# Kernel tuning notes

Hardware: AMD Instinct MI355X
Metric: run time of the kernel (lower is better)

The kernel has to match this reference:

```python
import jax, jax.numpy as jnp
import numpy as np

B, S = 256, 32          # sequence layout for the final (b, s, 1) reshape
BATCH = B * S           # 8192 flattened rows processed per call
IN, U, OUT = 32, 128, 1 # sensory inputs, interneurons, motor outputs
UNFOLDS = 6             # semi-implicit ODE solver unfolds


def _syn_sigmoid(v, mu, sigma):
    # v: [B, P]; mu, sigma: [P, Q] -> [B, P, Q] per-synapse gate
    return jax.nn.sigmoid(sigma * (v[:, :, None] - mu))


def setup_inputs() -> dict:
    key = jax.random.key(0)
    ks = jax.random.split(key, 12)
    inputs = jax.random.normal(ks[0], (BATCH, IN), dtype=jnp.float32)
    state = jax.random.normal(ks[1], (BATCH, U), dtype=jnp.float32)
    # adjacency in {-1, 0, 1} (wiring polarity), baked into W / erev as in _get_variables
    sens_adj = jax.random.randint(ks[2], (IN, U), -1, 2).astype(jnp.float32)
    adj = jax.random.randint(ks[3], (U, U), -1, 2).astype(jnp.float32)
    sensory_mu = jax.random.uniform(ks[4], (IN, U)) * 0.5 + 0.3
    sensory_sigma = jax.random.uniform(ks[5], (IN, U)) * 5.0 + 3.0
    # NOTE: original applies +w_init_min OUTSIDE the |adj| mask; reproduced faithfully
    sensory_W = jnp.abs(sens_adj) * jax.random.uniform(ks[6], (IN, U)) * 0.9 + 0.1
    sensory_erev = sens_adj  # erev_init_factor = 1
    mu = jax.random.uniform(ks[7], (U, U)) * 0.5 + 0.3
    sigma = jax.random.uniform(ks[8], (U, U)) * 5.0 + 3.0
    W = jnp.abs(adj) * jax.random.uniform(ks[9], (U, U)) * 0.9 + 0.1
    erev = adj
    vleak = jax.random.uniform(ks[10], (U,)) * 0.4 - 0.2
    gleak = jnp.ones((U,), jnp.float32)        # gleak_init_min == gleak_init_max == 1
    cm_t = jnp.ones((U,), jnp.float32) * 0.5    # cm_init_min == cm_init_max == 0.5
    in_w = jnp.ones((IN,), jnp.float32)         # affine input mapping (init ones/zeros)
    in_b = jnp.zeros((IN,), jnp.float32)
    out_w = jnp.ones((OUT,), jnp.float32)       # affine output mapping
    out_b = jnp.zeros((OUT,), jnp.float32)
    return dict(inputs=inputs, state=state, sensory_mu=sensory_mu,
                sensory_sigma=sensory_sigma, sensory_W=sensory_W,
                sensory_erev=sensory_erev, mu=mu, sigma=sigma, W=W, erev=erev,
                vleak=vleak, gleak=gleak, cm_t=cm_t, in_w=in_w, in_b=in_b,
                out_w=out_w, out_b=out_b, b=B, s=S)


def reference(inputs, state, sensory_mu, sensory_sigma, sensory_W, sensory_erev,
              mu, sigma, W, erev, vleak, gleak, cm_t, in_w, in_b, out_w, out_b,
              b, s):
    x = inputs * in_w + in_b                                   # _map_inputs (Affine)
    # sensory synapse activations, computed once: [BATCH, IN, U]
    sa = sensory_W * _syn_sigmoid(x, sensory_mu, sensory_sigma)
    w_num_s = jnp.sum(sa * sensory_erev, axis=1)               # [BATCH, U]
    w_den_s = jnp.sum(sa, axis=1)                              # [BATCH, U]

    def step(v, _):
        wa = W * _syn_sigmoid(v, mu, sigma)                    # [BATCH, U, U]
        w_num = jnp.sum(wa * erev, axis=1) + w_num_s
        w_den = jnp.sum(wa, axis=1) + w_den_s
        v_new = (cm_t * v + gleak * vleak + w_num) / (cm_t + gleak + w_den)
        return v_new, None

    v, _ = jax.lax.scan(step, state, None, length=UNFOLDS)
    outputs = (v[:, :OUT] * out_w + out_b).reshape(b, s, 1)    # _map_outputs
    return outputs, v
```

## Files before the change

kernel.cpp:

```cpp
#include <hip/hip_runtime.h>

#define NIN 32
#define NU  128
#define RPB 8
#define NQ  4
#define UNFOLDS 6
#define LOG2E 1.44269504088896340736f

typedef float float4v __attribute__((ext_vector_type(4)));

#define SPN (NIN * NU)
#define RPN (NU * NU)

__global__ void pack_params(const float* __restrict__ mu,
                            const float* __restrict__ sig,
                            const float* __restrict__ W,
                            const float* __restrict__ erev,
                            float4v* __restrict__ out, int n) {
    int idx = blockIdx.x * blockDim.x + threadIdx.x;
    if (idx < n) {
        float sg = sig[idx];
        float s2 = -LOG2E * sg;
        float sm2 = -s2 * mu[idx];
        float Wv = W[idx];
        float We = Wv * erev[idx];
        out[idx] = (float4v){s2, sm2, We, Wv};
    }
}

__global__ __launch_bounds__(512, 8)
void wormnet_main(const float* __restrict__ inputs,
                  const float* __restrict__ state,
                  const float4v* __restrict__ sp,
                  const float4v* __restrict__ rp,
                  const float* __restrict__ vleak,
                  const float* __restrict__ gleak,
                  const float* __restrict__ cm_t,
                  const float* __restrict__ in_w, const float* __restrict__ in_b,
                  const float* __restrict__ out_w, const float* __restrict__ out_b,
                  float* __restrict__ out_y,
                  float* __restrict__ out_v)
{
    __shared__ __align__(16) float xs[NIN * RPB];
    __shared__ __align__(16) float vs[NU * RPB];
    __shared__ float rn[RPB][NQ][NU];
    __shared__ float rd[RPB][NQ][NU];

    const int tid  = threadIdx.x;
    const int j    = tid & (NU - 1);
    const int q    = tid >> 7;
    const int base = blockIdx.x * RPB;
    const int u0   = q * 2;

    if (tid < NIN * RPB) {
        int i = tid & (NIN - 1);
        int r = tid >> 5;
        xs[i * RPB + r] = inputs[(base + r) * NIN + i] * in_w[i] + in_b[i];
    }
    float vold[2];
    #pragma unroll
    for (int k = 0; k < 2; ++k) {
        float v = state[(base + u0 + k) * NU + j];
        vold[k] = v;
        vs[j * RPB + u0 + k] = v;
    }
    __syncthreads();

    float numS[RPB], denS[RPB];
    #pragma unroll
    for (int r = 0; r < RPB; ++r) { numS[r] = 0.0f; denS[r] = 0.0f; }
    {
        const float4v* pp = sp + q * (NIN / NQ) * NU + j;
        #pragma unroll 2
        for (int ii = 0; ii < NIN / NQ; ++ii) {
            const int i = q * (NIN / NQ) + ii;
            float4v p = pp[0]; pp += NU;
            float4v xa = *(const float4v*)&xs[i * RPB];
            float4v xb = *(const float4v*)&xs[i * RPB + 4];
            float a[RPB];
            #pragma unroll
            for (int r = 0; r < 4; ++r) {
                a[r]     = 1.0f + __builtin_amdgcn_exp2f(__builtin_fmaf(p.x, xa[r], p.y));
                a[r + 4] = 1.0f + __builtin_amdgcn_exp2f(__builtin_fmaf(p.x, xb[r], p.y));
            }
            #pragma unroll
            for (int w = 0; w < RPB / 2; ++w) {
                float rq = __builtin_amdgcn_rcpf(a[2*w] * a[2*w+1]);
                float s0 = rq * a[2*w+1];
                float s1 = rq * a[2*w];
                numS[2*w]   = __builtin_fmaf(p.z, s0, numS[2*w]);
                denS[2*w]   = __builtin_fmaf(p.w, s0, denS[2*w]);
                numS[2*w+1] = __builtin_fmaf(p.z, s1, numS[2*w+1]);
                denS[2*w+1] = __builtin_fmaf(p.w, s1, denS[2*w+1]);
            }
        }
    }

    const float cm = cm_t[j];
    const float gl = gleak[j];
    const float glvl = gl * vleak[j];
    const float cg = cm + gl;

    for (int u = 0; u < UNFOLDS; ++u) {
        float num[RPB], den[RPB];
        #pragma unroll
        for (int r = 0; r < RPB; ++r) { num[r] = numS[r]; den[r] = denS[r]; }

        const float4v* pp = rp + q * (NU / NQ) * NU + j;
        #pragma unroll 2
        for (int ii = 0; ii < NU / NQ; ++ii) {
            const int i = q * (NU / NQ) + ii;
            float4v p = pp[0]; pp += NU;
            float4v va = *(const float4v*)&vs[i * RPB];
            float4v vb = *(const float4v*)&vs[i * RPB + 4];
            float a[RPB];
            #pragma unroll
            for (int r = 0; r < 4; ++r) {
                a[r]     = 1.0f + __builtin_amdgcn_exp2f(__builtin_fmaf(p.x, va[r], p.y));
                a[r + 4] = 1.0f + __builtin_amdgcn_exp2f(__builtin_fmaf(p.x, vb[r], p.y));
            }
            #pragma unroll
            for (int w = 0; w < RPB / 2; ++w) {
                float rq = __builtin_amdgcn_rcpf(a[2*w] * a[2*w+1]);
                float s0 = rq * a[2*w+1];
                float s1 = rq * a[2*w];
                num[2*w]   = __builtin_fmaf(p.z, s0, num[2*w]);
                den[2*w]   = __builtin_fmaf(p.w, s0, den[2*w]);
                num[2*w+1] = __builtin_fmaf(p.z, s1, num[2*w+1]);
                den[2*w+1] = __builtin_fmaf(p.w, s1, den[2*w+1]);
            }
        }

        #pragma unroll
        for (int r = 0; r < RPB; ++r) {
            rn[r][q][j] = num[r];
            rd[r][q][j] = den[r];
        }
        __syncthreads();

        #pragma unroll
        for (int k = 0; k < 2; ++k) {
            const int r = u0 + k;
            float tn = rn[r][0][j] + rn[r][1][j] + rn[r][2][j] + rn[r][3][j];
            float td = rd[r][0][j] + rd[r][1][j] + rd[r][2][j] + rd[r][3][j];
            float vn = (__builtin_fmaf(cm, vold[k], glvl) + tn)
                       * __builtin_amdgcn_rcpf(cg + td);
            vold[k] = vn;
            vs[j * RPB + r] = vn;
        }
        __syncthreads();
    }

    #pragma unroll
    for (int k = 0; k < 2; ++k) {
        out_v[(base + u0 + k) * NU + j] = vold[k];
    }
    if (j == 0) {
        const float ow = out_w[0], ob = out_b[0];
        #pragma unroll
        for (int k = 0; k < 2; ++k) {
            out_y[base + u0 + k] = __builtin_fmaf(vold[k], ow, ob);
        }
    }
}

extern "C" void kernel_launch(void* const* d_in, const int* in_sizes, int n_in,
                              void* d_out, int out_size, void* d_ws, size_t ws_size,
                              hipStream_t stream) {
    const float* inputs  = (const float*)d_in[0];
    const float* state   = (const float*)d_in[1];
    const float* smu     = (const float*)d_in[2];
    const float* ssig    = (const float*)d_in[3];
    const float* sW      = (const float*)d_in[4];
    const float* serev   = (const float*)d_in[5];
    const float* rmu     = (const float*)d_in[6];
    const float* rsig    = (const float*)d_in[7];
    const float* rW      = (const float*)d_in[8];
    const float* rerev   = (const float*)d_in[9];
    const float* vleak   = (const float*)d_in[10];
    const float* gleak   = (const float*)d_in[11];
    const float* cm_t    = (const float*)d_in[12];
    const float* in_w    = (const float*)d_in[13];
    const float* in_b    = (const float*)d_in[14];
    const float* out_w   = (const float*)d_in[15];
    const float* out_b   = (const float*)d_in[16];

    const int batch = in_sizes[1] / NU;
    float* out_y = (float*)d_out;
    float* out_v = (float*)d_out + batch;

    float4v* sp = (float4v*)d_ws;
    float4v* rp = sp + SPN;

    hipLaunchKernelGGL(pack_params, dim3((SPN + 255) / 256), dim3(256), 0, stream,
                       smu, ssig, sW, serev, sp, SPN);
    hipLaunchKernelGGL(pack_params, dim3((RPN + 255) / 256), dim3(256), 0, stream,
                       rmu, rsig, rW, rerev, rp, RPN);

    dim3 grid(batch / RPB), block(NU * NQ);
    hipLaunchKernelGGL(wormnet_main, grid, block, 0, stream,
                       inputs, state, sp, rp,
                       vleak, gleak, cm_t, in_w, in_b, out_w, out_b,
                       out_y, out_v);
}
```

Measured before the change: 267.6 us.

## Halve rows per block and simplify sigmoid pair evaluation

Rows per block drop from 8 to 4, so each of the 4 thread quarters owns one batch row instead of two, and the grid doubles. The sigmoid pair trick is rewritten as an EVAL_PAIR macro that folds the 1+e adds into FMAs, and the unroll pragmas rise to 4. The aim is lower register pressure and more waves in flight, at the cost of reloading the packed parameters twice as often across blocks and more block overhead.

```diff
diff --git a/kernel.cpp b/kernel.cpp
--- a/kernel.cpp
+++ b/kernel.cpp
@@ -2,7 +2,7 @@
 
 #define NIN 32
 #define NU  128
-#define RPB 8
+#define RPB 4
 #define NQ  4
 #define UNFOLDS 6
 #define LOG2E 1.44269504088896340736f
@@ -28,6 +28,21 @@
     }
 }
 
+#define EVAL_PAIR(p, v0, v1, n0, d0, n1, d1)                                   \
+    {                                                                          \
+        float e0 = __builtin_amdgcn_exp2f(__builtin_fmaf((p).x, (v0), (p).y)); \
+        float e1 = __builtin_amdgcn_exp2f(__builtin_fmaf((p).x, (v1), (p).y)); \
+        float a1 = 1.0f + e1;                                                  \
+        float P  = __builtin_fmaf(e0, a1, a1);                                 \
+        float rq = __builtin_amdgcn_rcpf(P);                                   \
+        float s0 = rq * a1;                                                    \
+        float s1 = __builtin_fmaf(rq, e0, rq);                                 \
+        (n0) = __builtin_fmaf((p).z, s0, (n0));                                \
+        (d0) = __builtin_fmaf((p).w, s0, (d0));                                \
+        (n1) = __builtin_fmaf((p).z, s1, (n1));                                \
+        (d1) = __builtin_fmaf((p).w, s1, (d1));                                \
+    }
+
 __global__ __launch_bounds__(512, 8)
 void wormnet_main(const float* __restrict__ inputs,
                   const float* __restrict__ state,
@@ -50,20 +65,14 @@
     const int j    = tid & (NU - 1);
     const int q    = tid >> 7;
     const int base = blockIdx.x * RPB;
-    const int u0   = q * 2;
 
     if (tid < NIN * RPB) {
         int i = tid & (NIN - 1);
         int r = tid >> 5;
         xs[i * RPB + r] = inputs[(base + r) * NIN + i] * in_w[i] + in_b[i];
     }
-    float vold[2];
-    #pragma unroll
-    for (int k = 0; k < 2; ++k) {
-        float v = state[(base + u0 + k) * NU + j];
-        vold[k] = v;
-        vs[j * RPB + u0 + k] = v;
-    }
+    float vold = state[(base + q) * NU + j];
+    vs[j * RPB + q] = vold;
     __syncthreads();
 
     float numS[RPB], denS[RPB];
@@ -71,28 +80,13 @@
     for (int r = 0; r < RPB; ++r) { numS[r] = 0.0f; denS[r] = 0.0f; }
     {
         const float4v* pp = sp + q * (NIN / NQ) * NU + j;
-        #pragma unroll 2
+        #pragma unroll 4
         for (int ii = 0; ii < NIN / NQ; ++ii) {
             const int i = q * (NIN / NQ) + ii;
             float4v p = pp[0]; pp += NU;
-            float4v xa = *(const float4v*)&xs[i * RPB];
-            float4v xb = *(const float4v*)&xs[i * RPB + 4];
-            float a[RPB];
-            #pragma unroll
-            for (int r = 0; r < 4; ++r) {
-                a[r]     = 1.0f + __builtin_amdgcn_exp2f(__builtin_fmaf(p.x, xa[r], p.y));
-                a[r + 4] = 1.0f + __builtin_amdgcn_exp2f(__builtin_fmaf(p.x, xb[r], p.y));
-            }
-            #pragma unroll
-            for (int w = 0; w < RPB / 2; ++w) {
-                float rq = __builtin_amdgcn_rcpf(a[2*w] * a[2*w+1]);
-                float s0 = rq * a[2*w+1];
-                float s1 = rq * a[2*w];
-                numS[2*w]   = __builtin_fmaf(p.z, s0, numS[2*w]);
-                denS[2*w]   = __builtin_fmaf(p.w, s0, denS[2*w]);
-                numS[2*w+1] = __builtin_fmaf(p.z, s1, numS[2*w+1]);
-                denS[2*w+1] = __builtin_fmaf(p.w, s1, denS[2*w+1]);
-            }
+            float4v xv = *(const float4v*)&xs[i * RPB];
+            EVAL_PAIR(p, xv[0], xv[1], numS[0], denS[0], numS[1], denS[1]);
+            EVAL_PAIR(p, xv[2], xv[3], numS[2], denS[2], numS[3], denS[3]);
         }
     }
 
@@ -107,28 +101,13 @@
         for (int r = 0; r < RPB; ++r) { num[r] = numS[r]; den[r] = denS[r]; }
 
         const float4v* pp = rp + q * (NU / NQ) * NU + j;
-        #pragma unroll 2
+        #pragma unroll 4
         for (int ii = 0; ii < NU / NQ; ++ii) {
             const int i = q * (NU / NQ) + ii;
             float4v p = pp[0]; pp += NU;
-            float4v va = *(const float4v*)&vs[i * RPB];
-            float4v vb = *(const float4v*)&vs[i * RPB + 4];
-            float a[RPB];
-            #pragma unroll
-            for (int r = 0; r < 4; ++r) {
-                a[r]     = 1.0f + __builtin_amdgcn_exp2f(__builtin_fmaf(p.x, va[r], p.y));
-                a[r + 4] = 1.0f + __builtin_amdgcn_exp2f(__builtin_fmaf(p.x, vb[r], p.y));
-            }
-            #pragma unroll
-            for (int w = 0; w < RPB / 2; ++w) {
-                float rq = __builtin_amdgcn_rcpf(a[2*w] * a[2*w+1]);
-                float s0 = rq * a[2*w+1];
-                float s1 = rq * a[2*w];
-                num[2*w]   = __builtin_fmaf(p.z, s0, num[2*w]);
-                den[2*w]   = __builtin_fmaf(p.w, s0, den[2*w]);
-                num[2*w+1] = __builtin_fmaf(p.z, s1, num[2*w+1]);
-                den[2*w+1] = __builtin_fmaf(p.w, s1, den[2*w+1]);
-            }
+            float4v vv = *(const float4v*)&vs[i * RPB];
+            EVAL_PAIR(p, vv[0], vv[1], num[0], den[0], num[1], den[1]);
+            EVAL_PAIR(p, vv[2], vv[3], num[2], den[2], num[3], den[3]);
         }
 
         #pragma unroll
@@ -138,29 +117,20 @@
         }
         __syncthreads();
 
-        #pragma unroll
-        for (int k = 0; k < 2; ++k) {
-            const int r = u0 + k;
-            float tn = rn[r][0][j] + rn[r][1][j] + rn[r][2][j] + rn[r][3][j];
-            float td = rd[r][0][j] + rd[r][1][j] + rd[r][2][j] + rd[r][3][j];
-            float vn = (__builtin_fmaf(cm, vold[k], glvl) + tn)
+        {
+            float tn = (rn[q][0][j] + rn[q][1][j]) + (rn[q][2][j] + rn[q][3][j]);
+            float td = (rd[q][0][j] + rd[q][1][j]) + (rd[q][2][j] + rd[q][3][j]);
+            float vn = (__builtin_fmaf(cm, vold, glvl) + tn)
                        * __builtin_amdgcn_rcpf(cg + td);
-            vold[k] = vn;
-            vs[j * RPB + r] = vn;
+            vold = vn;
+            vs[j * RPB + q] = vn;
         }
         __syncthreads();
     }
 
-    #pragma unroll
-    for (int k = 0; k < 2; ++k) {
-        out_v[(base + u0 + k) * NU + j] = vold[k];
-    }
+    out_v[(base + q) * NU + j] = vold;
     if (j == 0) {
-        const float ow = out_w[0], ob = out_b[0];
-        #pragma unroll
-        for (int k = 0; k < 2; ++k) {
-            out_y[base + u0 + k] = __builtin_fmaf(vold[k], ow, ob);
-        }
+        out_y[base + q] = __builtin_fmaf(vold, out_w[0], out_b[0]);
     }
 }
 
```

New measurement: 274.7 us. 1.03x slower.
